# Kernel optimization log

Hardware: AMD Instinct MI355X
Metric: run time of the kernel (lower is better)

The kernel has to match this reference:

```python
import jax, jax.numpy as jnp
import numpy as np

H = 2048      # hidden_size
NH = 16       # num_attention_heads
HD = H // NH  # head_dim = 128
B, S = 2, 2048
ROPE_BASE = 10000.0


def setup_inputs() -> dict:
    key = jax.random.key(0)
    ks = jax.random.split(key, 9)
    init = 0.02
    inp = {
        "hidden_states": jax.random.normal(ks[0], (B, S, H), dtype=jnp.float32),
        # torch nn.Linear weights are [out_features, in_features]
        "wq": jax.random.normal(ks[1], (H, H), dtype=jnp.float32) * init,
        "bq": jnp.zeros((H,), dtype=jnp.float32),
        "wk": jax.random.normal(ks[2], (H, H), dtype=jnp.float32) * init,
        "bk": jnp.zeros((H,), dtype=jnp.float32),
        "wv": jax.random.normal(ks[3], (H, H), dtype=jnp.float32) * init,
        "bv": jnp.zeros((H,), dtype=jnp.float32),
        "wo": jax.random.normal(ks[4], (H, H), dtype=jnp.float32) * init,
        "bo": jnp.zeros((H,), dtype=jnp.float32),
    }
    return inp


def _rope_cos_sin(seq_len, dim, dtype):
    # standard RoPE tables: [seq_len, dim]
    inv_freq = 1.0 / (ROPE_BASE ** (jnp.arange(0, dim, 2, dtype=jnp.float32) / dim))
    freqs = jnp.arange(seq_len, dtype=jnp.float32)[:, None] * inv_freq[None, :]
    emb = jnp.concatenate([freqs, freqs], axis=-1)  # [S, dim]
    return jnp.cos(emb).astype(dtype), jnp.sin(emb).astype(dtype)


def _rotate_half(x):
    half = x.shape[-1] // 2
    return jnp.concatenate([-x[..., half:], x[..., :half]], axis=-1)


def reference(hidden_states, wq, bq, wk, bk, wv, bv, wo, bo):
    b, s, h = hidden_states.shape
    scale = HD ** -0.5

    def proj(x, w, bias):
        y = jnp.einsum("bsh,oh->bso", x, w) + bias
        # -> [b, nh, s, hd]
        return y.reshape(b, s, NH, HD).transpose(0, 2, 1, 3)

    q = proj(hidden_states, wq, bq)
    k = proj(hidden_states, wk, bk)
    v = proj(hidden_states, wv, bv)

    # rotary embeddings on q, k
    cos, sin = _rope_cos_sin(s, HD, q.dtype)  # [s, hd]
    q = q * cos + _rotate_half(q) * sin
    k = k * cos + _rotate_half(k) * sin

    # causal additive mask [s, s]
    mask = jnp.triu(jnp.full((s, s), -1e9, dtype=q.dtype), k=1)

    scores = jnp.einsum("bhqd,bhkd->bhqk", q, k) * scale + mask
    probs = jax.nn.softmax(scores, axis=-1)
    attn = jnp.einsum("bhqk,bhkd->bhqd", probs, v)
    attn = attn.transpose(0, 2, 1, 3).reshape(b, s, h)
    out = jnp.einsum("bsh,oh->bso", attn, wo) + bo
    return out
```

## Files before the change

kernel.cpp:

```cpp
#include <hip/hip_runtime.h>

typedef unsigned short u16;
typedef __attribute__((ext_vector_type(8))) __bf16 bf16x8;
typedef __attribute__((ext_vector_type(4))) float f32x4;
typedef __attribute__((ext_vector_type(4))) u16 u16x4;
typedef __attribute__((ext_vector_type(8))) u16 u16x8;

constexpr int S = 2048;
constexpr int H = 2048;
constexpr int NH = 16;
constexpr int HD = 128;
constexpr int M = 4096;
constexpr float SCALE = 0.08838834764831845f;

__device__ __forceinline__ u16 f2bf(float f) {
  union { float f; unsigned u; } v; v.f = f;
  unsigned r = v.u + 0x7fffu + ((v.u >> 16) & 1u);
  return (u16)(r >> 16);
}
__device__ __forceinline__ float bf2f(u16 u) {
  union { unsigned u; float f; } v; v.u = ((unsigned)u) << 16;
  return v.f;
}
__device__ __forceinline__ unsigned cvt_pk_bf16(float lo, float hi) {
  unsigned r;
  asm("v_cvt_pk_bf16_f32 %0, %1, %2" : "=v"(r) : "v"(lo), "v"(hi));
  return r;
}
__device__ __forceinline__ f32x4 MFMA16(bf16x8 a, bf16x8 b, f32x4 c) {
  return __builtin_amdgcn_mfma_f32_16x16x32_bf16(a, b, c, 0, 0, 0);
}

__device__ __forceinline__ void gld16(const u16* g, u16* l) {
  __builtin_amdgcn_global_load_lds(
      (const __attribute__((address_space(1))) void*)g,
      (__attribute__((address_space(3))) void*)l, 16, 0, 0);
}

#define SBAR  { __builtin_amdgcn_sched_barrier(0); __builtin_amdgcn_s_barrier(); __builtin_amdgcn_sched_barrier(0); }
#define LGKM0 { asm volatile("s_waitcnt lgkmcnt(0)" ::: "memory"); __builtin_amdgcn_sched_barrier(0); }

__global__ __launch_bounds__(256) void cast_kernel(const float* __restrict__ in,
                                                   u16* __restrict__ out, int n) {
  int i = (blockIdx.x * 256 + threadIdx.x) * 4;
  if (i >= n) return;
  float4 v = *(const float4*)(in + i);
  u16x4 o;
  o[0] = f2bf(v.x); o[1] = f2bf(v.y); o[2] = f2bf(v.z); o[3] = f2bf(v.w);
  *(u16x4*)(out + i) = o;
}

__global__ __launch_bounds__(256) void cast4_kernel(const float* __restrict__ i0,
                                                    const float* __restrict__ i1,
                                                    const float* __restrict__ i2,
                                                    const float* __restrict__ i3,
                                                    u16* o0, u16* o1, u16* o2, u16* o3) {
  const float* in; u16* out;
  switch (blockIdx.y) {
    case 0: in = i0; out = o0; break;
    case 1: in = i1; out = o1; break;
    case 2: in = i2; out = o2; break;
    default: in = i3; out = o3; break;
  }
  int i = (blockIdx.x * 256 + threadIdx.x) * 4;
  float4 v = *(const float4*)(in + i);
  u16x4 o;
  o[0] = f2bf(v.x); o[1] = f2bf(v.y); o[2] = f2bf(v.z); o[3] = f2bf(v.w);
  *(u16x4*)(out + i) = o;
}

__global__ __launch_bounds__(256) void concat_bias_k(const float* __restrict__ bq,
                                                     const float* __restrict__ bk,
                                                     const float* __restrict__ bv,
                                                     float* __restrict__ bqkv) {
  int i = blockIdx.x * 256 + threadIdx.x;
  const float* src = (i < 2048) ? bq : (i < 4096) ? bk : bv;
  bqkv[i] = src[i & 2047];
}

__global__ __launch_bounds__(256) void rope_table_k(float* __restrict__ tab) {
  int i = blockIdx.x * 256 + threadIdx.x;
  if (i >= S * 64) return;
  int s = i >> 6, d = i & 63;
  float freq = expf(-(float)d * (9.210340371976184f / 64.f));
  float ang = (float)s * freq;
  tab[i * 2]     = cosf(ang);
  tab[i * 2 + 1] = sinf(ang);
}

__global__ __launch_bounds__(256) void rope_apply2_k(u16* __restrict__ Qb, u16* __restrict__ Kb,
                                                     const float* __restrict__ tab) {
  u16* X = blockIdx.y ? Kb : Qb;
  const float sc = blockIdx.y ? 1.f : SCALE;
  int i = blockIdx.x * 256 + threadIdx.x;
  int j0 = (i & 7) * 8;
  int h  = (i >> 3) & 15;
  int m  = i >> 7;
  int s  = m & (S - 1);
  u16* p = X + (size_t)m * H + h * HD;
  u16x8 lo = *(u16x8*)(p + j0);
  u16x8 hi = *(u16x8*)(p + 64 + j0);
  u16x8 nlo, nhi;
  const float* tb = tab + ((size_t)s * 64 + j0) * 2;
  #pragma unroll
  for (int j = 0; j < 8; ++j) {
    float c = tb[j * 2], sn = tb[j * 2 + 1];
    float xl = bf2f(lo[j]), xh = bf2f(hi[j]);
    nlo[j] = f2bf((xl * c - xh * sn) * sc);
    nhi[j] = f2bf((xh * c + xl * sn) * sc);
  }
  *(u16x8*)(p + j0) = nlo;
  *(u16x8*)(p + 64 + j0) = nhi;
}

template<int NW, int EMODE>
__device__ __forceinline__ void gemm_body(const u16* __restrict__ A,
                                          const u16* __restrict__ Bw,
                                          const float* __restrict__ bias,
                                          void* __restrict__ out0, void* __restrict__ out1,
                                          void* __restrict__ out2,
                                          int brow, int bcol,
                                          u16* AsL, u16* BsL) {
  const int t = threadIdx.x;
  const int w = t >> 6, l = t & 63;
  const int wr = w >> 2, wc = w & 3;
  const int lr = l & 15, lg = l >> 4;
  const int swz = lr & 7;

  f32x4 acc[8][NW] = {};
  bf16x8 af[4], b0[NW], b1[NW];

  const int sr = t >> 3, sj = t & 7;

  auto STAGE_A = [&](int BUF, int HALF, int TILE) {
    u16* d = AsL + BUF * (256 * 64) + HALF * (128 * 64);
    const u16* sp = A + (size_t)(brow + HALF * 128) * H + TILE * 64;
    gld16(sp + (size_t)sr * H        + ((sj ^ (sr & 7)) * 8), d + t * 8);
    gld16(sp + (size_t)(64 + sr) * H + ((sj ^ (sr & 7)) * 8), d + (512 + t) * 8);
  };
  auto STAGE_B = [&](int BUF, int TILE) {
    u16* d = BsL + BUF * (NW * 64 * 64);
    const u16* sp = Bw + (size_t)bcol * H + TILE * 64;
    #pragma unroll
    for (int i = 0; i < NW; ++i)
      gld16(sp + (size_t)(i * 64 + sr) * H + ((sj ^ (sr & 7)) * 8),
            d + (i * 512 + t) * 8);
  };
  auto LDA = [&](int BUF, int KH, int MB) {
    const u16* base = AsL + BUF * (256 * 64) + (wr * 128 + MB * 16 + lr) * 64;
    #pragma unroll
    for (int i = 0; i < 4; ++i)
      af[i] = *(const bf16x8*)(base + i * (16 * 64) + (((KH * 4 + lg) ^ swz) * 8));
  };
  auto LDB = [&](int BUF, int KH, bf16x8* bb) {
    const u16* base = BsL + BUF * (NW * 64 * 64) + (wc * (NW * 16) + lr) * 64;
    #pragma unroll
    for (int n = 0; n < NW; ++n)
      bb[n] = *(const bf16x8*)(base + n * (16 * 64) + (((KH * 4 + lg) ^ swz) * 8));
  };
  auto MM = [&](int MB, bf16x8* bb) {
    __builtin_amdgcn_s_setprio(1);
    #pragma unroll
    for (int i = 0; i < 4; ++i)
      #pragma unroll
      for (int n = 0; n < NW; ++n)
        acc[MB + i][n] = MFMA16(af[i], bb[n], acc[MB + i][n]);
    __builtin_amdgcn_s_setprio(0);
  };
  auto GATE = [&]() {
    if constexpr (NW == 3) { asm volatile("s_waitcnt vmcnt(3)" ::: "memory"); }
    else                   { asm volatile("s_waitcnt vmcnt(2)" ::: "memory"); }
  };

  STAGE_A(0, 0, 0); STAGE_A(0, 1, 0);
  STAGE_B(0, 0);
  STAGE_B(1, 1);
  GATE();
  SBAR;

  for (int J = 0; J < 16; ++J) {
    const int u = 2 * J;
    const bool more = (J < 15);
    LDA(0, 0, 0); LDB(0, 0, b0);
    STAGE_A(1, 0, u + 1);
    SBAR; LGKM0; MM(0, b0); SBAR;
    LDA(0, 0, 4);
    STAGE_A(1, 1, u + 1);
    SBAR; LGKM0; MM(4, b0); SBAR;
    LDA(0, 1, 0); LDB(0, 1, b1);
    SBAR; LGKM0; MM(0, b1); SBAR;
    LDA(0, 1, 4);
    if (more) STAGE_B(0, u + 2);
    SBAR; LGKM0; MM(4, b1);
    if (more) { GATE(); } else { asm volatile("s_waitcnt vmcnt(0)" ::: "memory"); }
    SBAR;
    LDA(1, 0, 0); LDB(1, 0, b0);
    if (more) STAGE_A(0, 0, u + 2);
    SBAR; LGKM0; MM(0, b0); SBAR;
    LDA(1, 0, 4);
    if (more) STAGE_A(0, 1, u + 2);
    SBAR; LGKM0; MM(4, b0); SBAR;
    LDA(1, 1, 0); LDB(1, 1, b1);
    SBAR; LGKM0; MM(0, b1); SBAR;
    LDA(1, 1, 4);
    if (more) STAGE_B(1, u + 3);
    SBAR; LGKM0; MM(4, b1);
    if (more) { GATE(); SBAR; }
  }

  #pragma unroll
  for (int m = 0; m < 8; ++m) {
    const int row0 = brow + wr * 128 + m * 16 + lg * 4;
    #pragma unroll
    for (int n = 0; n < NW; ++n) {
      const int gcol0 = bcol + wc * (NW * 16) + n * 16;
      const float bv = bias[gcol0 + lr];
      if constexpr (EMODE == 0) {
        float* C = (float*)out0;
        #pragma unroll
        for (int r = 0; r < 4; ++r)
          C[(size_t)(row0 + r) * H + gcol0 + lr] = acc[m][n][r] + bv;
      } else {
        const int sel = gcol0 >> 11;
        const int col = (gcol0 & 2047) + lr;
        if (sel < 2) {
          u16* C = sel ? (u16*)out1 : (u16*)out0;
          #pragma unroll
          for (int r = 0; r < 4; ++r)
            C[(size_t)(row0 + r) * H + col] = f2bf(acc[m][n][r] + bv);
        } else {
          const int hh = col >> 7, d = col & 127;
          const int b = row0 >> 11, s0 = row0 & (S - 1);
          u16x4 pk;
          #pragma unroll
          for (int r = 0; r < 4; ++r) pk[r] = f2bf(acc[m][n][r] + bv);
          *(u16x4*)((u16*)out2 + ((size_t)((b * 16 + hh) * 128 + d)) * S + s0) = pk;
        }
      }
    }
  }
}

__global__ __launch_bounds__(512, 2) void gemm_qkv8(const u16* __restrict__ xb,
                                                    const u16* __restrict__ wqkv,
                                                    const float* __restrict__ bqkv,
                                                    u16* Qb, u16* Kb, u16* Vt) {
  __shared__ u16 AsL[2 * 256 * 64];
  __shared__ u16 BsL[2 * 192 * 64];
  const int id = blockIdx.x;
  const int xcd = id & 7, sid = id >> 3;
  const int bx = xcd * 4 + (sid & 3), by = sid >> 2;
  gemm_body<3, 3>(xb, wqkv, bqkv, Qb, Kb, Vt, by * 256, bx * 192, AsL, BsL);
}

__global__ __launch_bounds__(512, 2) void gemm_o8(const u16* __restrict__ A,
                                                  const u16* __restrict__ W,
                                                  const float* __restrict__ bias,
                                                  float* __restrict__ C) {
  __shared__ u16 AsL[2 * 256 * 64];
  __shared__ u16 BsL[2 * 128 * 64];
  const int id = blockIdx.x;
  const int xcd = id & 7, sid = id >> 3;
  const int bx = xcd * 2 + (sid & 1), by = sid >> 1;
  gemm_body<2, 0>(A, W, bias, C, nullptr, nullptr, by * 256, bx * 128, AsL, BsL);
}

__global__ __launch_bounds__(256) void attn_fwd(const u16* __restrict__ Q,
                                                const u16* __restrict__ Kx,
                                                const u16* __restrict__ Vt,
                                                u16* __restrict__ O) {
  const int id = blockIdx.x;
  const int xcd = id & 7, slot = id >> 3;
  const int bh = (slot >> 4) * 8 + xcd;
  const int pid = slot & 15;
  const int b = bh >> 4, h = bh & 15;
  const int t = threadIdx.x, w = t >> 6, l = t & 63;
  const int lr = l & 15, lg = l >> 4;
  const int swz = lr & 7;

  __shared__ u16 Ks[2][64 * 128];
  __shared__ u16 Vs[2][128 * 64];
  __shared__ u16 P_lds[4][16 * 64];
  u16* pw = &P_lds[w][0];

  const u16* kbase = Kx + (size_t)(b * S) * H + h * HD;
  const u16* vbase = Vt + (size_t)bh * HD * S;

  auto stageK = [&](int bf, int k0) {
    #pragma unroll
    for (int it = 0; it < 4; ++it) {
      int c = it * 256 + t;
      int row = c >> 4, j = c & 15;
      gld16(kbase + (size_t)(k0 + row) * H + ((j ^ (row & 7)) * 8), &Ks[bf][0] + c * 8);
    }
  };
  auto stageV = [&](int bf, int k0) {
    #pragma unroll
    for (int it = 0; it < 4; ++it) {
      int c = it * 256 + t;
      int row = c >> 3, j = c & 7;
      gld16(vbase + (size_t)row * S + k0 + ((j ^ (row & 7)) * 8), &Vs[bf][0] + c * 8);
    }
  };

  int cur = 0;
  for (int qi = 0; qi < 2; ++qi) {
    const int qt = qi ? pid : (31 - pid);
    const int q0 = qt * 64 + w * 16;

    bf16x8 qa[4];
    const u16* qbase = Q + (size_t)(b * S + q0 + lr) * H + h * HD;
    #pragma unroll
    for (int ks = 0; ks < 4; ++ks)
      qa[ks] = *(const bf16x8*)(qbase + ks * 32 + lg * 8);

    f32x4 acc[8] = {};
    float mrun[4], lrun[4];
    #pragma unroll
    for (int r = 0; r < 4; ++r) { mrun[r] = -1e30f; lrun[r] = 0.f; }

    __syncthreads();
    stageK(cur, 0);
    stageV(cur, 0);
    __syncthreads();

    for (int kt = 0; kt <= qt; ++kt) {
      if (kt < qt) {
        stageK(cur ^ 1, (kt + 1) * 64);
        stageV(cur ^ 1, (kt + 1) * 64);
      }
      const u16* kl = &Ks[cur][0];
      const u16* vl = &Vs[cur][0];

      f32x4 sc[4] = {};
      __builtin_amdgcn_s_setprio(1);
      #pragma unroll
      for (int ks = 0; ks < 4; ++ks) {
        #pragma unroll
        for (int f = 0; f < 4; ++f) {
          bf16x8 kf = *(const bf16x8*)(kl + (f * 16 + lr) * 128 + (((ks * 4 + lg) ^ swz) * 8));
          sc[f] = __builtin_amdgcn_mfma_f32_16x16x32_bf16(qa[ks], kf, sc[f], 0, 0, 0);
        }
      }
      __builtin_amdgcn_s_setprio(0);
      const bool diag = (kt == qt);
      float p[4][4];
      #pragma unroll
      for (int f = 0; f < 4; ++f)
        #pragma unroll
        for (int r = 0; r < 4; ++r) {
          float v = sc[f][r];
          if (diag && (f * 16 + lr > w * 16 + lg * 4 + r)) v = -1e30f;
          p[f][r] = v;
        }
      float mx[4];
      #pragma unroll
      for (int r = 0; r < 4; ++r) {
        float m0 = fmaxf(fmaxf(p[0][r], p[1][r]), fmaxf(p[2][r], p[3][r]));
        m0 = fmaxf(m0, __shfl_xor(m0, 1));
        m0 = fmaxf(m0, __shfl_xor(m0, 2));
        m0 = fmaxf(m0, __shfl_xor(m0, 4));
        m0 = fmaxf(m0, __shfl_xor(m0, 8));
        mx[r] = m0;
      }
      bool grow = (mx[0] > mrun[0] + 8.f) || (mx[1] > mrun[1] + 8.f) ||
                  (mx[2] > mrun[2] + 8.f) || (mx[3] > mrun[3] + 8.f);
      if (__any(grow)) {
        float resc[4];
        #pragma unroll
        for (int r = 0; r < 4; ++r) {
          float mnew = fmaxf(mrun[r], mx[r]);
          resc[r] = __expf(mrun[r] - mnew);
          mrun[r] = mnew;
          lrun[r] *= resc[r];
        }
        #pragma unroll
        for (int fd = 0; fd < 8; ++fd) {
          f32x4 a = acc[fd];
          a[0] *= resc[0]; a[1] *= resc[1]; a[2] *= resc[2]; a[3] *= resc[3];
          acc[fd] = a;
        }
      }
      #pragma unroll
      for (int r = 0; r < 4; ++r) {
        float sum = 0.f;
        #pragma unroll
        for (int f = 0; f < 4; ++f) {
          float e = __expf(p[f][r] - mrun[r]);
          p[f][r] = e;
          sum += e;
        }
        sum += __shfl_xor(sum, 1);
        sum += __shfl_xor(sum, 2);
        sum += __shfl_xor(sum, 4);
        sum += __shfl_xor(sum, 8);
        lrun[r] += sum;
      }
      {
        const int r0 = lg * 4;
        #pragma unroll
        for (int f = 0; f < 4; ++f) {
          const int col = f * 16 + lr;
          unsigned w01 = cvt_pk_bf16(p[f][0], p[f][1]);
          unsigned w23 = cvt_pk_bf16(p[f][2], p[f][3]);
          pw[(r0 + 0) * 64 + (col ^ (((r0 + 0) & 7) << 3))] = (u16)(w01 & 0xffffu);
          pw[(r0 + 1) * 64 + (col ^ (((r0 + 1) & 7) << 3))] = (u16)(w01 >> 16);
          pw[(r0 + 2) * 64 + (col ^ (((r0 + 2) & 7) << 3))] = (u16)(w23 & 0xffffu);
          pw[(r0 + 3) * 64 + (col ^ (((r0 + 3) & 7) << 3))] = (u16)(w23 >> 16);
        }
      }
      __builtin_amdgcn_s_setprio(1);
      #pragma unroll
      for (int ks = 0; ks < 2; ++ks) {
        int col0 = ks * 32 + lg * 8;
        bf16x8 pa = *(const bf16x8*)(pw + lr * 64 + (col0 ^ (swz << 3)));
        #pragma unroll
        for (int fd = 0; fd < 8; ++fd) {
          bf16x8 vb = *(const bf16x8*)(vl + (fd * 16 + lr) * 64 + (((ks * 4 + lg) ^ swz) * 8));
          acc[fd] = __builtin_amdgcn_mfma_f32_16x16x32_bf16(pa, vb, acc[fd], 0, 0, 0);
        }
      }
      __builtin_amdgcn_s_setprio(0);
      __syncthreads();
      cur ^= 1;
    }

    u16* ob = O + (size_t)(b * S + q0 + lg * 4) * H + h * HD;
    #pragma unroll
    for (int r = 0; r < 4; ++r) {
      float inv = 1.f / lrun[r];
      #pragma unroll
      for (int fd = 0; fd < 8; ++fd)
        ob[(size_t)r * H + fd * 16 + lr] = f2bf(acc[fd][r] * inv);
    }
  }
}

extern "C" void kernel_launch(void* const* d_in, const int* in_sizes, int n_in,
                              void* d_out, int out_size, void* d_ws, size_t ws_size,
                              hipStream_t stream) {
  const float* x  = (const float*)d_in[0];
  const float* wq = (const float*)d_in[1];
  const float* bq = (const float*)d_in[2];
  const float* wk = (const float*)d_in[3];
  const float* bk = (const float*)d_in[4];
  const float* wv = (const float*)d_in[5];
  const float* bv = (const float*)d_in[6];
  const float* wo = (const float*)d_in[7];
  const float* bo = (const float*)d_in[8];

  char* ws = (char*)d_ws;
  u16*   xb    = (u16*)(ws);
  u16*   wqkvb = (u16*)(ws + (16ull << 20));
  u16*   wob   = (u16*)(ws + (40ull << 20));
  u16*   Qb    = (u16*)(ws + (48ull << 20));
  u16*   Kb    = (u16*)(ws + (64ull << 20));
  u16*   Vt    = (u16*)(ws + (80ull << 20));
  u16*   Ob    = (u16*)(ws + (96ull << 20));
  float* tab   = (float*)(ws + (112ull << 20));
  float* bqkv  = (float*)(ws + (113ull << 20));

  cast_kernel<<<M * H / 1024, 256, 0, stream>>>(x, xb, M * H);
  cast4_kernel<<<dim3(H * H / 1024, 4), 256, 0, stream>>>(
      wq, wk, wv, wo, wqkvb, wqkvb + (size_t)H * H, wqkvb + 2ull * H * H, wob);
  rope_table_k<<<(S * 64 + 255) / 256, 256, 0, stream>>>(tab);
  concat_bias_k<<<24, 256, 0, stream>>>(bq, bk, bv, bqkv);

  gemm_qkv8<<<512, 512, 0, stream>>>(xb, wqkvb, bqkv, Qb, Kb, Vt);

  rope_apply2_k<<<dim3(M * NH * 8 / 256, 2), 256, 0, stream>>>(Qb, Kb, tab);

  attn_fwd<<<512, 256, 0, stream>>>(Qb, Kb, Vt, Ob);

  gemm_o8<<<256, 512, 0, stream>>>(Ob, wob, bo, (float*)d_out);
}
```

Measured before the change: 275.5 us.

## Fuse RoPE into QKV GEMM epilogue with 256-wide tiles

Replaces the 192-column QKV GEMM and the separate RoPE kernel with a 256x256-tile GEMM whose epilogue applies the bias, the rotary embedding and the softmax scale. Each wave pairs with its neighbour through LDS to fetch the rotate-half partner column. This removes a full read-modify-write pass over Q and K and one kernel launch. In exchange the epilogue gains LDS round trips and barriers, and the launch shrinks to 384 blocks, which may hurt load balance.

```diff
diff --git a/kernel.cpp b/kernel.cpp
--- a/kernel.cpp
+++ b/kernel.cpp
@@ -88,37 +88,171 @@
   tab[i * 2 + 1] = sinf(ang);
 }
 
-__global__ __launch_bounds__(256) void rope_apply2_k(u16* __restrict__ Qb, u16* __restrict__ Kb,
-                                                     const float* __restrict__ tab) {
-  u16* X = blockIdx.y ? Kb : Qb;
-  const float sc = blockIdx.y ? 1.f : SCALE;
-  int i = blockIdx.x * 256 + threadIdx.x;
-  int j0 = (i & 7) * 8;
-  int h  = (i >> 3) & 15;
-  int m  = i >> 7;
-  int s  = m & (S - 1);
-  u16* p = X + (size_t)m * H + h * HD;
-  u16x8 lo = *(u16x8*)(p + j0);
-  u16x8 hi = *(u16x8*)(p + 64 + j0);
-  u16x8 nlo, nhi;
-  const float* tb = tab + ((size_t)s * 64 + j0) * 2;
-  #pragma unroll
-  for (int j = 0; j < 8; ++j) {
-    float c = tb[j * 2], sn = tb[j * 2 + 1];
-    float xl = bf2f(lo[j]), xh = bf2f(hi[j]);
-    nlo[j] = f2bf((xl * c - xh * sn) * sc);
-    nhi[j] = f2bf((xh * c + xl * sn) * sc);
+__global__ __launch_bounds__(512, 2) void gemm_qkv4(const u16* __restrict__ A,
+                                                    const u16* __restrict__ Bw,
+                                                    const float* __restrict__ bias,
+                                                    const float* __restrict__ tab,
+                                                    u16* __restrict__ Qb,
+                                                    u16* __restrict__ Kb,
+                                                    u16* __restrict__ Vt) {
+  __shared__ u16 AsL[2 * 256 * 64];
+  __shared__ u16 BsL[2 * 256 * 64];
+
+  const int id = blockIdx.x;
+  const int xcd = id & 7, sid = id >> 3;
+  const int bx = xcd * 3 + (sid % 3);
+  const int by = sid / 3;
+  const int brow = by * 256, bcol = bx * 256;
+  const int sel = bcol >> 11;
+
+  const int t = threadIdx.x;
+  const int w = t >> 6, l = t & 63;
+  const int wr = w >> 2, wc = w & 3;
+  const int lr = l & 15, lg = l >> 4;
+  const int swz = lr & 7;
+
+  f32x4 acc[8][4] = {};
+  bf16x8 af[4], b0[4], b1[4];
+
+  const int sr = t >> 3, sj = t & 7;
+
+  auto STAGE_A = [&](int BUF, int HALF, int TILE) {
+    u16* d = AsL + BUF * (256 * 64) + HALF * (128 * 64);
+    const u16* sp = A + (size_t)(brow + HALF * 128) * H + TILE * 64;
+    gld16(sp + (size_t)sr * H        + ((sj ^ (sr & 7)) * 8), d + t * 8);
+    gld16(sp + (size_t)(64 + sr) * H + ((sj ^ (sr & 7)) * 8), d + (512 + t) * 8);
+  };
+  auto STAGE_B = [&](int BUF, int TILE) {
+    u16* d = BsL + BUF * (256 * 64);
+    const u16* sp = Bw + (size_t)bcol * H + TILE * 64;
+    #pragma unroll
+    for (int i = 0; i < 4; ++i)
+      gld16(sp + (size_t)(i * 64 + sr) * H + ((sj ^ (sr & 7)) * 8),
+            d + (i * 512 + t) * 8);
+  };
+  auto LDA = [&](int BUF, int KH, int MB) {
+    const u16* base = AsL + BUF * (256 * 64) + (wr * 128 + MB * 16 + lr) * 64;
+    #pragma unroll
+    for (int i = 0; i < 4; ++i)
+      af[i] = *(const bf16x8*)(base + i * (16 * 64) + (((KH * 4 + lg) ^ swz) * 8));
+  };
+  auto LDB = [&](int BUF, int KH, bf16x8* bb) {
+    const u16* base = BsL + BUF * (256 * 64) + (wc * 64 + lr) * 64;
+    #pragma unroll
+    for (int n = 0; n < 4; ++n)
+      bb[n] = *(const bf16x8*)(base + n * (16 * 64) + (((KH * 4 + lg) ^ swz) * 8));
+  };
+  auto MM = [&](int MB, bf16x8* bb) {
+    __builtin_amdgcn_s_setprio(1);
+    #pragma unroll
+    for (int i = 0; i < 4; ++i)
+      #pragma unroll
+      for (int n = 0; n < 4; ++n)
+        acc[MB + i][n] = MFMA16(af[i], bb[n], acc[MB + i][n]);
+    __builtin_amdgcn_s_setprio(0);
+  };
+
+  STAGE_A(0, 0, 0); STAGE_A(0, 1, 0);
+  STAGE_B(0, 0);
+  STAGE_B(1, 1);
+  asm volatile("s_waitcnt vmcnt(4)" ::: "memory");
+  SBAR;
+
+  for (int J = 0; J < 16; ++J) {
+    const int u = 2 * J;
+    const bool more = (J < 15);
+    LDA(0, 0, 0); LDB(0, 0, b0);
+    STAGE_A(1, 0, u + 1);
+    SBAR; LGKM0; MM(0, b0); SBAR;
+
+    LDA(0, 0, 4);
+    STAGE_A(1, 1, u + 1);
+    SBAR; LGKM0; MM(4, b0); SBAR;
+
+    LDA(0, 1, 0); LDB(0, 1, b1);
+    SBAR; LGKM0; MM(0, b1); SBAR;
+
+    LDA(0, 1, 4);
+    if (more) STAGE_B(0, u + 2);
+    SBAR; LGKM0; MM(4, b1);
+    if (more) { asm volatile("s_waitcnt vmcnt(4)" ::: "memory"); }
+    else      { asm volatile("s_waitcnt vmcnt(0)" ::: "memory"); }
+    SBAR;
+    LDA(1, 0, 0); LDB(1, 0, b0);
+    if (more) STAGE_A(0, 0, u + 2);
+    SBAR; LGKM0; MM(0, b0); SBAR;
+
+    LDA(1, 0, 4);
+    if (more) STAGE_A(0, 1, u + 2);
+    SBAR; LGKM0; MM(4, b0); SBAR;
+
+    LDA(1, 1, 0); LDB(1, 1, b1);
+    SBAR; LGKM0; MM(0, b1); SBAR;
+
+    LDA(1, 1, 4);
+    if (more) STAGE_B(1, u + 3);
+    SBAR; LGKM0; MM(4, b1);
+    if (more) { asm volatile("s_waitcnt vmcnt(4)" ::: "memory"); SBAR; }
   }
-  *(u16x8*)(p + j0) = nlo;
-  *(u16x8*)(p + 64 + j0) = nhi;
-}
-
-template<int NW, int EMODE>
+
+  if (sel < 2) {
+    float* lf = (float*)AsL;
+    u16* Cq = sel ? Kb : Qb;
+    const float scl = sel ? 1.f : SCALE;
+    #pragma unroll
+    for (int m = 0; m < 8; ++m) {
+      __syncthreads();
+      float mine[4][4];
+      #pragma unroll
+      for (int n = 0; n < 4; ++n) {
+        const float bv = bias[bcol + wc * 64 + n * 16 + lr];
+        #pragma unroll
+        for (int r = 0; r < 4; ++r) {
+          mine[n][r] = acc[m][n][r] + bv;
+          lf[w * (16 * 66) + (lg * 4 + r) * 66 + n * 16 + lr] = mine[n][r];
+        }
+      }
+      __syncthreads();
+      #pragma unroll
+      for (int n = 0; n < 4; ++n) {
+        const int j = n * 16 + lr;
+        const int hcol = ((bcol & 2047) + wc * 64 + j);
+        #pragma unroll
+        for (int r = 0; r < 4; ++r) {
+          const int row = brow + wr * 128 + m * 16 + lg * 4 + r;
+          const int s = row & (S - 1);
+          float pr = lf[(w ^ 1) * (16 * 66) + (lg * 4 + r) * 66 + j];
+          float2 cs = ((const float2*)tab)[s * 64 + j];
+          float out = (wc & 1) ? (mine[n][r] * cs.x + pr * cs.y)
+                               : (mine[n][r] * cs.x - pr * cs.y);
+          Cq[(size_t)row * H + hcol] = f2bf(out * scl);
+        }
+      }
+    }
+  } else {
+    #pragma unroll
+    for (int m = 0; m < 8; ++m) {
+      const int row0 = brow + wr * 128 + m * 16 + lg * 4;
+      #pragma unroll
+      for (int n = 0; n < 4; ++n) {
+        const int col = (bcol & 2047) + wc * 64 + n * 16 + lr;
+        const float bv = bias[bcol + wc * 64 + n * 16 + lr];
+        const int hh = col >> 7, d = col & 127;
+        const int b = row0 >> 11, s0 = row0 & (S - 1);
+        u16x4 pk;
+        #pragma unroll
+        for (int r = 0; r < 4; ++r) pk[r] = f2bf(acc[m][n][r] + bv);
+        *(u16x4*)(Vt + ((size_t)((b * 16 + hh) * 128 + d)) * S + s0) = pk;
+      }
+    }
+  }
+}
+
+template<int NW>
 __device__ __forceinline__ void gemm_body(const u16* __restrict__ A,
                                           const u16* __restrict__ Bw,
                                           const float* __restrict__ bias,
-                                          void* __restrict__ out0, void* __restrict__ out1,
-                                          void* __restrict__ out2,
+                                          float* __restrict__ Cout,
                                           int brow, int bcol,
                                           u16* AsL, u16* BsL) {
   const int t = threadIdx.x;
@@ -168,8 +302,7 @@
     __builtin_amdgcn_s_setprio(0);
   };
   auto GATE = [&]() {
-    if constexpr (NW == 3) { asm volatile("s_waitcnt vmcnt(3)" ::: "memory"); }
-    else                   { asm volatile("s_waitcnt vmcnt(2)" ::: "memory"); }
+    asm volatile("s_waitcnt vmcnt(2)" ::: "memory");
   };
 
   STAGE_A(0, 0, 0); STAGE_A(0, 1, 0);
@@ -213,44 +346,13 @@
     const int row0 = brow + wr * 128 + m * 16 + lg * 4;
     #pragma unroll
     for (int n = 0; n < NW; ++n) {
-      const int gcol0 = bcol + wc * (NW * 16) + n * 16;
-      const float bv = bias[gcol0 + lr];
-      if constexpr (EMODE == 0) {
-        float* C = (float*)out0;
-        #pragma unroll
-        for (int r = 0; r < 4; ++r)
-          C[(size_t)(row0 + r) * H + gcol0 + lr] = acc[m][n][r] + bv;
-      } else {
-        const int sel = gcol0 >> 11;
-        const int col = (gcol0 & 2047) + lr;
-        if (sel < 2) {
-          u16* C = sel ? (u16*)out1 : (u16*)out0;
-          #pragma unroll
-          for (int r = 0; r < 4; ++r)
-            C[(size_t)(row0 + r) * H + col] = f2bf(acc[m][n][r] + bv);
-        } else {
-          const int hh = col >> 7, d = col & 127;
-          const int b = row0 >> 11, s0 = row0 & (S - 1);
-          u16x4 pk;
-          #pragma unroll
-          for (int r = 0; r < 4; ++r) pk[r] = f2bf(acc[m][n][r] + bv);
-          *(u16x4*)((u16*)out2 + ((size_t)((b * 16 + hh) * 128 + d)) * S + s0) = pk;
-        }
-      }
+      const int col = bcol + wc * (NW * 16) + n * 16 + lr;
+      const float bv = bias[col];
+      #pragma unroll
+      for (int r = 0; r < 4; ++r)
+        Cout[(size_t)(row0 + r) * H + col] = acc[m][n][r] + bv;
     }
   }
-}
-
-__global__ __launch_bounds__(512, 2) void gemm_qkv8(const u16* __restrict__ xb,
-                                                    const u16* __restrict__ wqkv,
-                                                    const float* __restrict__ bqkv,
-                                                    u16* Qb, u16* Kb, u16* Vt) {
-  __shared__ u16 AsL[2 * 256 * 64];
-  __shared__ u16 BsL[2 * 192 * 64];
-  const int id = blockIdx.x;
-  const int xcd = id & 7, sid = id >> 3;
-  const int bx = xcd * 4 + (sid & 3), by = sid >> 2;
-  gemm_body<3, 3>(xb, wqkv, bqkv, Qb, Kb, Vt, by * 256, bx * 192, AsL, BsL);
 }
 
 __global__ __launch_bounds__(512, 2) void gemm_o8(const u16* __restrict__ A,
@@ -262,7 +364,7 @@
   const int id = blockIdx.x;
   const int xcd = id & 7, sid = id >> 3;
   const int bx = xcd * 2 + (sid & 1), by = sid >> 1;
-  gemm_body<2, 0>(A, W, bias, C, nullptr, nullptr, by * 256, bx * 128, AsL, BsL);
+  gemm_body<2>(A, W, bias, C, by * 256, bx * 128, AsL, BsL);
 }
 
 __global__ __launch_bounds__(256) void attn_fwd(const u16* __restrict__ Q,
@@ -466,9 +568,7 @@
   rope_table_k<<<(S * 64 + 255) / 256, 256, 0, stream>>>(tab);
   concat_bias_k<<<24, 256, 0, stream>>>(bq, bk, bv, bqkv);
 
-  gemm_qkv8<<<512, 512, 0, stream>>>(xb, wqkvb, bqkv, Qb, Kb, Vt);
-
-  rope_apply2_k<<<dim3(M * NH * 8 / 256, 2), 256, 0, stream>>>(Qb, Kb, tab);
+  gemm_qkv4<<<384, 512, 0, stream>>>(xb, wqkvb, bqkv, tab, Qb, Kb, Vt);
 
   attn_fwd<<<512, 256, 0, stream>>>(Qb, Kb, Vt, Ob);
 
```

Result: slower. 296.9 us (+7.8%).

## Fuse RoPE into QKV GEMM epilogue via interleaved weight rows; merge prep kernels

Applied to the files above, without the earlier changes.

The Q and K weight and bias rows are permuted during the bf16 cast so that each rotary pair (d, d+64) lands in adjacent output columns. RoPE and the softmax scale are then applied in the QKV GEMM epilogue, using a lane-xor shuffle and a cos/sin table lookup. This removes the separate rope pass, which read and rewrote Q and K in global memory. The four prep launches (x cast, weight casts, rope table, bias concat) are also merged into one kernel to cut launch overhead. The epilogue pays for this with extra shuffles and table loads, and Q and K are now stored in a permuted head-dim order that stays consistent between them.

```diff
diff --git a/kernel.cpp b/kernel.cpp
--- a/kernel.cpp
+++ b/kernel.cpp
@@ -40,83 +40,83 @@
 #define SBAR  { __builtin_amdgcn_sched_barrier(0); __builtin_amdgcn_s_barrier(); __builtin_amdgcn_sched_barrier(0); }
 #define LGKM0 { asm volatile("s_waitcnt lgkmcnt(0)" ::: "memory"); __builtin_amdgcn_sched_barrier(0); }
 
-__global__ __launch_bounds__(256) void cast_kernel(const float* __restrict__ in,
-                                                   u16* __restrict__ out, int n) {
-  int i = (blockIdx.x * 256 + threadIdx.x) * 4;
-  if (i >= n) return;
-  float4 v = *(const float4*)(in + i);
-  u16x4 o;
-  o[0] = f2bf(v.x); o[1] = f2bf(v.y); o[2] = f2bf(v.z); o[3] = f2bf(v.w);
-  *(u16x4*)(out + i) = o;
-}
-
-__global__ __launch_bounds__(256) void cast4_kernel(const float* __restrict__ i0,
-                                                    const float* __restrict__ i1,
-                                                    const float* __restrict__ i2,
-                                                    const float* __restrict__ i3,
-                                                    u16* o0, u16* o1, u16* o2, u16* o3) {
-  const float* in; u16* out;
-  switch (blockIdx.y) {
-    case 0: in = i0; out = o0; break;
-    case 1: in = i1; out = o1; break;
-    case 2: in = i2; out = o2; break;
-    default: in = i3; out = o3; break;
-  }
-  int i = (blockIdx.x * 256 + threadIdx.x) * 4;
-  float4 v = *(const float4*)(in + i);
-  u16x4 o;
-  o[0] = f2bf(v.x); o[1] = f2bf(v.y); o[2] = f2bf(v.z); o[3] = f2bf(v.w);
-  *(u16x4*)(out + i) = o;
-}
-
-__global__ __launch_bounds__(256) void concat_bias_k(const float* __restrict__ bq,
-                                                     const float* __restrict__ bk,
-                                                     const float* __restrict__ bv,
-                                                     float* __restrict__ bqkv) {
-  int i = blockIdx.x * 256 + threadIdx.x;
-  const float* src = (i < 2048) ? bq : (i < 4096) ? bk : bv;
-  bqkv[i] = src[i & 2047];
-}
-
-__global__ __launch_bounds__(256) void rope_table_k(float* __restrict__ tab) {
-  int i = blockIdx.x * 256 + threadIdx.x;
-  if (i >= S * 64) return;
-  int s = i >> 6, d = i & 63;
-  float freq = expf(-(float)d * (9.210340371976184f / 64.f));
-  float ang = (float)s * freq;
-  tab[i * 2]     = cosf(ang);
-  tab[i * 2 + 1] = sinf(ang);
-}
-
-__global__ __launch_bounds__(256) void rope_apply2_k(u16* __restrict__ Qb, u16* __restrict__ Kb,
-                                                     const float* __restrict__ tab) {
-  u16* X = blockIdx.y ? Kb : Qb;
-  const float sc = blockIdx.y ? 1.f : SCALE;
-  int i = blockIdx.x * 256 + threadIdx.x;
-  int j0 = (i & 7) * 8;
-  int h  = (i >> 3) & 15;
-  int m  = i >> 7;
-  int s  = m & (S - 1);
-  u16* p = X + (size_t)m * H + h * HD;
-  u16x8 lo = *(u16x8*)(p + j0);
-  u16x8 hi = *(u16x8*)(p + 64 + j0);
-  u16x8 nlo, nhi;
-  const float* tb = tab + ((size_t)s * 64 + j0) * 2;
-  #pragma unroll
-  for (int j = 0; j < 8; ++j) {
-    float c = tb[j * 2], sn = tb[j * 2 + 1];
-    float xl = bf2f(lo[j]), xh = bf2f(hi[j]);
-    nlo[j] = f2bf((xl * c - xh * sn) * sc);
-    nhi[j] = f2bf((xh * c + xl * sn) * sc);
-  }
-  *(u16x8*)(p + j0) = nlo;
-  *(u16x8*)(p + 64 + j0) = nhi;
+__global__ __launch_bounds__(256) void prep_kernel(const float* __restrict__ x,
+                                                   const float* __restrict__ wq,
+                                                   const float* __restrict__ wk,
+                                                   const float* __restrict__ wv,
+                                                   const float* __restrict__ wo,
+                                                   const float* __restrict__ bq,
+                                                   const float* __restrict__ bk,
+                                                   const float* __restrict__ bv,
+                                                   u16* __restrict__ xb,
+                                                   u16* __restrict__ wqkvb,
+                                                   u16* __restrict__ wob,
+                                                   float* __restrict__ tab,
+                                                   float* __restrict__ bqkv) {
+  const int NX = (M * H) / 1024;
+  const int NW = (H * H) / 1024;
+  int bid = blockIdx.x;
+  if (bid < NX) {
+    int i = (bid * 256 + threadIdx.x) * 4;
+    float4 v = *(const float4*)(x + i);
+    u16x4 o;
+    o[0] = f2bf(v.x); o[1] = f2bf(v.y); o[2] = f2bf(v.z); o[3] = f2bf(v.w);
+    *(u16x4*)(xb + i) = o;
+    return;
+  }
+  bid -= NX;
+  if (bid < 4 * NW) {
+    const int z = bid / NW, lb = bid % NW;
+    const float* in;
+    u16* out;
+    switch (z) {
+      case 0: in = wq; out = wqkvb; break;
+      case 1: in = wk; out = wqkvb + (size_t)H * H; break;
+      case 2: in = wv; out = wqkvb + 2ull * H * H; break;
+      default: in = wo; out = wob; break;
+    }
+    int i = (lb * 256 + threadIdx.x) * 4;
+    int ro = i >> 11, cb = i & 2047;
+    int rin = ro;
+    if (z < 2) {
+      int nd = ro & 127;
+      int od = (nd & 1) ? (nd >> 1) + 64 : (nd >> 1);
+      rin = (ro & ~127) | od;
+    }
+    float4 v = *(const float4*)(in + (size_t)rin * H + cb);
+    u16x4 o;
+    o[0] = f2bf(v.x); o[1] = f2bf(v.y); o[2] = f2bf(v.z); o[3] = f2bf(v.w);
+    *(u16x4*)(out + i) = o;
+    return;
+  }
+  bid -= 4 * NW;
+  if (bid < 512) {
+    int i = bid * 256 + threadIdx.x;
+    int s = i >> 6, d = i & 63;
+    float freq = expf(-(float)d * (9.210340371976184f / 64.f));
+    float ang = (float)s * freq;
+    tab[i * 2]     = cosf(ang);
+    tab[i * 2 + 1] = sinf(ang);
+    return;
+  }
+  bid -= 512;
+  int i = bid * 256 + threadIdx.x;
+  if (i < 4096) {
+    const float* src = (i < 2048) ? bq : bk;
+    int base = i & 2047;
+    int nd = base & 127;
+    int od = (nd & 1) ? (nd >> 1) + 64 : (nd >> 1);
+    bqkv[i] = src[(base & ~127) | od];
+  } else {
+    bqkv[i] = bv[i & 2047];
+  }
 }
 
 template<int NW, int EMODE>
 __device__ __forceinline__ void gemm_body(const u16* __restrict__ A,
                                           const u16* __restrict__ Bw,
                                           const float* __restrict__ bias,
+                                          const float* __restrict__ tab,
                                           void* __restrict__ out0, void* __restrict__ out1,
                                           void* __restrict__ out2,
                                           int brow, int bcol,
@@ -214,26 +214,36 @@
     #pragma unroll
     for (int n = 0; n < NW; ++n) {
       const int gcol0 = bcol + wc * (NW * 16) + n * 16;
-      const float bv = bias[gcol0 + lr];
+      const float bv2 = bias[gcol0 + lr];
       if constexpr (EMODE == 0) {
         float* C = (float*)out0;
         #pragma unroll
         for (int r = 0; r < 4; ++r)
-          C[(size_t)(row0 + r) * H + gcol0 + lr] = acc[m][n][r] + bv;
+          C[(size_t)(row0 + r) * H + gcol0 + lr] = acc[m][n][r] + bv2;
       } else {
         const int sel = gcol0 >> 11;
         const int col = (gcol0 & 2047) + lr;
         if (sel < 2) {
-          u16* C = sel ? (u16*)out1 : (u16*)out0;
+          u16* Cq = sel ? (u16*)out1 : (u16*)out0;
+          const float scl = sel ? 1.f : SCALE;
+          const int d = (col & 127) >> 1;
           #pragma unroll
-          for (int r = 0; r < 4; ++r)
-            C[(size_t)(row0 + r) * H + col] = f2bf(acc[m][n][r] + bv);
+          for (int r = 0; r < 4; ++r) {
+            const int row = row0 + r;
+            const int s = row & (S - 1);
+            float xv = acc[m][n][r] + bv2;
+            float pr = __shfl_xor(xv, 1);
+            float2 cs = ((const float2*)tab)[s * 64 + d];
+            float o = (lr & 1) ? (xv * cs.x + pr * cs.y)
+                               : (xv * cs.x - pr * cs.y);
+            Cq[(size_t)row * H + col] = f2bf(o * scl);
+          }
         } else {
           const int hh = col >> 7, d = col & 127;
           const int b = row0 >> 11, s0 = row0 & (S - 1);
           u16x4 pk;
           #pragma unroll
-          for (int r = 0; r < 4; ++r) pk[r] = f2bf(acc[m][n][r] + bv);
+          for (int r = 0; r < 4; ++r) pk[r] = f2bf(acc[m][n][r] + bv2);
           *(u16x4*)((u16*)out2 + ((size_t)((b * 16 + hh) * 128 + d)) * S + s0) = pk;
         }
       }
@@ -244,13 +254,14 @@
 __global__ __launch_bounds__(512, 2) void gemm_qkv8(const u16* __restrict__ xb,
                                                     const u16* __restrict__ wqkv,
                                                     const float* __restrict__ bqkv,
+                                                    const float* __restrict__ tab,
                                                     u16* Qb, u16* Kb, u16* Vt) {
   __shared__ u16 AsL[2 * 256 * 64];
   __shared__ u16 BsL[2 * 192 * 64];
   const int id = blockIdx.x;
   const int xcd = id & 7, sid = id >> 3;
   const int bx = xcd * 4 + (sid & 3), by = sid >> 2;
-  gemm_body<3, 3>(xb, wqkv, bqkv, Qb, Kb, Vt, by * 256, bx * 192, AsL, BsL);
+  gemm_body<3, 3>(xb, wqkv, bqkv, tab, Qb, Kb, Vt, by * 256, bx * 192, AsL, BsL);
 }
 
 __global__ __launch_bounds__(512, 2) void gemm_o8(const u16* __restrict__ A,
@@ -262,7 +273,7 @@
   const int id = blockIdx.x;
   const int xcd = id & 7, sid = id >> 3;
   const int bx = xcd * 2 + (sid & 1), by = sid >> 1;
-  gemm_body<2, 0>(A, W, bias, C, nullptr, nullptr, by * 256, bx * 128, AsL, BsL);
+  gemm_body<2, 0>(A, W, bias, nullptr, C, nullptr, nullptr, by * 256, bx * 128, AsL, BsL);
 }
 
 __global__ __launch_bounds__(256) void attn_fwd(const u16* __restrict__ Q,
@@ -460,15 +471,11 @@
   float* tab   = (float*)(ws + (112ull << 20));
   float* bqkv  = (float*)(ws + (113ull << 20));
 
-  cast_kernel<<<M * H / 1024, 256, 0, stream>>>(x, xb, M * H);
-  cast4_kernel<<<dim3(H * H / 1024, 4), 256, 0, stream>>>(
-      wq, wk, wv, wo, wqkvb, wqkvb + (size_t)H * H, wqkvb + 2ull * H * H, wob);
-  rope_table_k<<<(S * 64 + 255) / 256, 256, 0, stream>>>(tab);
-  concat_bias_k<<<24, 256, 0, stream>>>(bq, bk, bv, bqkv);
-
-  gemm_qkv8<<<512, 512, 0, stream>>>(xb, wqkvb, bqkv, Qb, Kb, Vt);
-
-  rope_apply2_k<<<dim3(M * NH * 8 / 256, 2), 256, 0, stream>>>(Qb, Kb, tab);
+  const int NPREP = (M * H) / 1024 + 4 * (H * H) / 1024 + 512 + 24;
+  prep_kernel<<<NPREP, 256, 0, stream>>>(x, wq, wk, wv, wo, bq, bk, bv,
+                                         xb, wqkvb, wob, tab, bqkv);
+
+  gemm_qkv8<<<512, 512, 0, stream>>>(xb, wqkvb, bqkv, tab, Qb, Kb, Vt);
 
   attn_fwd<<<512, 256, 0, stream>>>(Qb, Kb, Vt, Ob);
 
```

Result: faster. 263.6 us (-4.3%).
